# Performance work log

Measured on AMD Instinct MI355X. Metric: run time of the kernel, lower is better.

## Reference

```python
import jax, jax.numpy as jnp
import numpy as np

N = 100000       # nodes
E = 800000       # edges (avg degree 8)
D_IN = 256
D_H = 128
K = 16           # cluster_num
LAMBDA1 = 1.0    # args.alphaH
LAMBDA2 = 0.5    # args.alphaO
GAMMA = 0.1      # args.step_size_gamma


def setup_inputs() -> dict:
    key = jax.random.key(0)
    ks = jax.random.split(key, 8)
    x = jax.random.normal(ks[0], (N, D_IN), jnp.float32)
    edge_index = jax.random.randint(ks[1], (2, E), 0, N, jnp.int32)
    # learned params (glorot-ish small init to keep Gram term numerically tame)
    W1 = jax.random.normal(ks[2], (D_IN, D_H), jnp.float32) * 0.002
    b1 = jnp.zeros((D_H,), jnp.float32)
    W2 = jax.random.normal(ks[3], (D_H, D_H), jnp.float32) * 0.01
    b2 = jnp.zeros((D_H,), jnp.float32)
    Wf = jax.random.normal(ks[4], (D_H, K), jnp.float32) * 0.05
    bf = jnp.zeros((K,), jnp.float32)
    return {"x": x, "edge_index": edge_index, "W1": W1, "b1": b1,
            "W2": W2, "b2": b2, "Wf": Wf, "bf": bf}


def _gcn_norm(edge_index, n):
    # add self loops, symmetric normalization D^-1/2 A D^-1/2 (PyG gcn_norm)
    loops = jnp.arange(n, dtype=edge_index.dtype)
    row = jnp.concatenate([edge_index[0], loops])   # source
    col = jnp.concatenate([edge_index[1], loops])   # target
    w = jnp.ones(row.shape[0], jnp.float32)
    deg = jax.ops.segment_sum(w, col, num_segments=n)
    dinv = jnp.where(deg > 0, jax.lax.rsqrt(jnp.maximum(deg, 1.0)), 0.0)
    return row, col, dinv[row] * w * dinv[col]


def _deprop_layer(x, W, b, row, col, w, n):
    x = x @ W                                               # lin (no bias)
    z = (1.0 - GAMMA * LAMBDA1 + GAMMA * LAMBDA2) * x
    # propagate: gather source features, scale by edge weight, scatter-add to target
    s = GAMMA * LAMBDA1 * jax.ops.segment_sum(w[:, None] * x[row], col, num_segments=n)
    # dense Gram correction: x @ (x^T x), d_h x d_h contraction
    t = GAMMA * LAMBDA2 * (x @ (x.T @ x))
    return jax.nn.relu(z + s - t + b)                       # bias add + ReLU


def reference(x, edge_index, W1, b1, W2, b2, Wf, bf):
    n = x.shape[0]
    row, col, w = _gcn_norm(edge_index, n)  # cached=True -> computed once, reused
    x = _deprop_layer(x, W1, b1, row, col, w, n)
    x = _deprop_layer(x, W2, b2, row, col, w, n)
    logits = x @ Wf + bf                    # fc; dropout is identity in eval mode
    return jax.nn.log_softmax(logits, axis=1)
```

## Files before the change

### kernel.cpp

```cpp
#include <hip/hip_runtime.h>

#define NNODES 100000
#define NEDGES 800000
#define DIN    256
#define DH     128
#define KCLS   16
#define SCAN_NBLK 98
#define GCH 64
#define GRAM_BLK 256

typedef unsigned short u16;
typedef short s16x8 __attribute__((ext_vector_type(8)));
typedef float f32x4 __attribute__((ext_vector_type(4)));

static constexpr float CZ = 0.95f;
static constexpr float CS = 0.10f;
static constexpr float CT = 0.05f;

__device__ __forceinline__ u16 f2b(float f) {
    unsigned u = __builtin_bit_cast(unsigned, f);
    return (u16)((u + 0x7FFFu + ((u >> 16) & 1u)) >> 16);
}
__device__ __forceinline__ float b2f(u16 b) {
    return __builtin_bit_cast(float, ((unsigned)b) << 16);
}
__device__ __forceinline__ s16x8 f2b8(float4 u0, float4 u1) {
    s16x8 v;
    v[0] = (short)f2b(u0.x); v[1] = (short)f2b(u0.y);
    v[2] = (short)f2b(u0.z); v[3] = (short)f2b(u0.w);
    v[4] = (short)f2b(u1.x); v[5] = (short)f2b(u1.y);
    v[6] = (short)f2b(u1.z); v[7] = (short)f2b(u1.w);
    return v;
}


__global__ __launch_bounds__(256) void zero_kernel(int* __restrict__ p) {
    int i = blockIdx.x * 256 + threadIdx.x;
    if (i < NNODES) p[i] = 0;
}

__global__ __launch_bounds__(256) void hist_kernel(const int* __restrict__ col, int* counts) {
    int i = blockIdx.x * 256 + threadIdx.x;
    if (i < NEDGES) atomicAdd(&counts[col[i]], 1);
}

__global__ __launch_bounds__(256) void dinv_kernel(const int* __restrict__ counts, float* dinv) {
    int i = blockIdx.x * 256 + threadIdx.x;
    if (i < NNODES) dinv[i] = rsqrtf((float)(counts[i] + 1));
}

__global__ __launch_bounds__(256) void scan1_kernel(const int* __restrict__ counts,
                                                    int* __restrict__ offsets, int* __restrict__ bsum) {
    __shared__ int ls[256];
    const int b = blockIdx.x, t = threadIdx.x;
    const int base = b * 1024 + t * 4;
    int v0 = (base + 0 < NNODES) ? counts[base + 0] : 0;
    int v1 = (base + 1 < NNODES) ? counts[base + 1] : 0;
    int v2 = (base + 2 < NNODES) ? counts[base + 2] : 0;
    int v3 = (base + 3 < NNODES) ? counts[base + 3] : 0;
    ls[t] = v0 + v1 + v2 + v3;
    __syncthreads();
    for (int off = 1; off < 256; off <<= 1) {
        int v = (t >= off) ? ls[t - off] : 0;
        __syncthreads();
        ls[t] += v;
        __syncthreads();
    }
    int excl = (t == 0) ? 0 : ls[t - 1];
    if (t == 255) bsum[b] = ls[255];
    if (base + 0 < NNODES) offsets[base + 0] = excl;
    if (base + 1 < NNODES) offsets[base + 1] = excl + v0;
    if (base + 2 < NNODES) offsets[base + 2] = excl + v0 + v1;
    if (base + 3 < NNODES) offsets[base + 3] = excl + v0 + v1 + v2;
}

__global__ __launch_bounds__(128) void scan2_kernel(int* bsum) {
    __shared__ int ls[128];
    const int t = threadIdx.x;
    int v = (t < SCAN_NBLK) ? bsum[t] : 0;
    ls[t] = v;
    __syncthreads();
    for (int off = 1; off < 128; off <<= 1) {
        int u = (t >= off) ? ls[t - off] : 0;
        __syncthreads();
        ls[t] += u;
        __syncthreads();
    }
    if (t < SCAN_NBLK) bsum[t] = ls[t] - v;
}

__global__ __launch_bounds__(256) void scan3_kernel(int* __restrict__ offsets, const int* __restrict__ bsum) {
    const int b = blockIdx.x, t = threadIdx.x;
    const int add = bsum[b];
    const int base = b * 1024 + t * 4;
    #pragma unroll
    for (int i = 0; i < 4; ++i)
        if (base + i < NNODES) offsets[base + i] += add;
    if (b == 0 && t == 0) offsets[NNODES] = NEDGES;
}

__global__ __launch_bounds__(256)
void fill_kernel(const int* __restrict__ row, const int* __restrict__ col,
                 const int* __restrict__ offsets, int* __restrict__ cursor,
                 int* __restrict__ eidx) {
    int e = blockIdx.x * 256 + threadIdx.x;
    if (e >= NEDGES) return;
    int c = col[e];
    int p = offsets[c] + atomicAdd(&cursor[c], 1);
    eidx[p] = row[e];
}


template<int KD>
__global__ __launch_bounds__(256)
void tr_w_kernel(const float* __restrict__ W, u16* __restrict__ Wt) {
    int idx = blockIdx.x * 256 + threadIdx.x;
    if (idx < 128 * KD) {
        int c = idx / KD, k = idx % KD;
        Wt[idx] = f2b(W[k * 128 + c]);
    }
}

template<int KD, int EPI, int AF, int WS>
__global__ __launch_bounds__(256, 4)
void mm_bt(const void* __restrict__ Avoid, const u16* __restrict__ Bt,
           u16* __restrict__ Out, const u16* __restrict__ Hb,
           const u16* __restrict__ Sb, const float* __restrict__ bias,
           const float* __restrict__ dinvp, u16* __restrict__ Hs,
           int nrows)
{
    __shared__ __align__(16) u16 as_[2][128 * 40];
    __shared__ __align__(16) u16 bs_[2][128 * 40];
    const int t = threadIdx.x;
    const int w = t >> 6, l = t & 63;
    const int l15 = l & 15, g = l >> 4;
    const int row0 = blockIdx.x * 128;

    const u16*   Ab = (const u16*)Avoid;
    const float* Af = (const float*)Avoid;

    const int sr = t >> 2, so = t & 3;
    int arow[2];
    arow[0] = min(row0 + sr,      nrows - 1);
    arow[1] = min(row0 + 64 + sr, nrows - 1);

    #pragma unroll
    for (int i = 0; i < 2; ++i) {
        s16x8 va;
        if (AF) {
            const float4* p = (const float4*)&Af[(size_t)arow[i] * KD + so * 8];
            va = f2b8(p[0], p[1]);
        } else {
            va = *(const s16x8*)&Ab[(size_t)arow[i] * KD + so * 8];
        }
        s16x8 vb = *(const s16x8*)&Bt[(size_t)(sr + i * 64) * KD + so * 8];
        *(s16x8*)&as_[0][(sr + i * 64) * 40 + so * 8] = va;
        *(s16x8*)&bs_[0][(sr + i * 64) * 40 + so * 8] = vb;
    }
    __syncthreads();

    f32x4 acc[2][8] = {};
    constexpr int NK = KD / 32;

    for (int kc = 0; kc < NK; ++kc) {
        const int buf = kc & 1;
        s16x8 va[2], vb[2];
        const bool pf = (kc + 1 < NK);
        if (pf) {
            const int k0 = (kc + 1) * 32;
            #pragma unroll
            for (int i = 0; i < 2; ++i) {
                if (AF) {
                    const float4* p = (const float4*)&Af[(size_t)arow[i] * KD + k0 + so * 8];
                    va[i] = f2b8(p[0], p[1]);
                } else {
                    va[i] = *(const s16x8*)&Ab[(size_t)arow[i] * KD + k0 + so * 8];
                }
                vb[i] = *(const s16x8*)&Bt[(size_t)(sr + i * 64) * KD + k0 + so * 8];
            }
        }
        s16x8 af0 = *(const s16x8*)&as_[buf][(w * 32 +      l15) * 40 + g * 8];
        s16x8 af1 = *(const s16x8*)&as_[buf][(w * 32 + 16 + l15) * 40 + g * 8];
        #pragma unroll
        for (int n = 0; n < 8; ++n) {
            s16x8 bfr = *(const s16x8*)&bs_[buf][(n * 16 + l15) * 40 + g * 8];
            acc[0][n] = __builtin_amdgcn_mfma_f32_16x16x32_bf16(af0, bfr, acc[0][n], 0, 0, 0);
            acc[1][n] = __builtin_amdgcn_mfma_f32_16x16x32_bf16(af1, bfr, acc[1][n], 0, 0, 0);
        }
        if (pf) {
            #pragma unroll
            for (int i = 0; i < 2; ++i) {
                *(s16x8*)&as_[buf ^ 1][(sr + i * 64) * 40 + so * 8] = va[i];
                *(s16x8*)&bs_[buf ^ 1][(sr + i * 64) * 40 + so * 8] = vb[i];
            }
        }
        __syncthreads();
    }

    float bv[8];
    if (EPI) {
        #pragma unroll
        for (int n = 0; n < 8; ++n) bv[n] = bias[n * 16 + l15];
    }
    #pragma unroll
    for (int m = 0; m < 2; ++m) {
        #pragma unroll
        for (int j = 0; j < 4; ++j) {
            int grow = row0 + w * 32 + m * 16 + g * 4 + j;
            if (grow < nrows) {
                size_t base = (size_t)grow * 128;
                float dv = WS ? dinvp[grow] : 0.f;
                #pragma unroll
                for (int n = 0; n < 8; ++n) {
                    int col = n * 16 + l15;
                    float v = acc[m][n][j];
                    if (EPI) {
                        float h = b2f(Hb[base + col]);
                        float s = b2f(Sb[base + col]);
                        v = fmaxf(CZ * h + CS * s - CT * v + bv[n], 0.f);
                    }
                    Out[base + col] = f2b(v);
                    if (WS) Hs[base + col] = f2b(dv * v);
                }
            }
        }
    }
}

__global__ __launch_bounds__(256)
void gram_gather(const u16* __restrict__ Hb, const u16* __restrict__ Hsb,
                 const float* __restrict__ dinv,
                 const int* __restrict__ offsets, const int* __restrict__ eidx,
                 float* __restrict__ P, u16* __restrict__ Sb, int nrows)
{
    __shared__ __align__(16) u16 ht[128 * GCH];
    const int t = threadIdx.x;

    if (blockIdx.x < GRAM_BLK) {
        const int bid = blockIdx.x;
        const int w = t >> 6, l = t & 63;
        const int l15 = l & 15, g = l >> 4;
        const int nch = (nrows + GCH - 1) / GCH;

        f32x4 acc[2][8] = {};
        const int sr = t >> 2, sq = t & 3;

        for (int ch = bid; ch < nch; ch += GRAM_BLK) {
            {
                int gr = ch * GCH + sr;
                #pragma unroll
                for (int i4 = 0; i4 < 4; ++i4) {
                    int c0 = sq * 32 + i4 * 8;
                    s16x8 v = {};
                    if (gr < nrows) v = *(const s16x8*)&Hb[(size_t)gr * DH + c0];
                    #pragma unroll
                    for (int i = 0; i < 8; ++i) {
                        int c = c0 + i;
                        ht[c * GCH + (sr ^ ((c & 7) << 3))] = (u16)v[i];
                    }
                }
            }
            __syncthreads();
            #pragma unroll
            for (int ks = 0; ks < 2; ++ks) {
                const int kx = (ks * 32 + g * 8) ^ ((l & 7) << 3);
                s16x8 a0 = *(const s16x8*)&ht[(w * 32 +      l15) * GCH + kx];
                s16x8 a1 = *(const s16x8*)&ht[(w * 32 + 16 + l15) * GCH + kx];
                #pragma unroll
                for (int n = 0; n < 8; ++n) {
                    s16x8 bfr = *(const s16x8*)&ht[(n * 16 + l15) * GCH + kx];
                    acc[0][n] = __builtin_amdgcn_mfma_f32_16x16x32_bf16(a0, bfr, acc[0][n], 0, 0, 0);
                    acc[1][n] = __builtin_amdgcn_mfma_f32_16x16x32_bf16(a1, bfr, acc[1][n], 0, 0, 0);
                }
            }
            __syncthreads();
        }

        float* Pb = P + (size_t)bid * (DH * DH);
        #pragma unroll
        for (int m = 0; m < 2; ++m)
            #pragma unroll
            for (int j = 0; j < 4; ++j) {
                int prow = w * 32 + m * 16 + g * 4 + j;
                #pragma unroll
                for (int n = 0; n < 8; ++n)
                    Pb[prow * DH + n * 16 + l15] = acc[m][n][j];
            }
    } else {
        const int grp = t >> 4;
        const int gl  = t & 15;
        const int node = (blockIdx.x - GRAM_BLK) * 16 + grp;
        if (node >= NNODES) return;
        const s16x8* Hs8 = (const s16x8*)Hsb;
        const float d = dinv[node];
        s16x8 hv = Hs8[(size_t)node * 16 + gl];
        float a[8];
        #pragma unroll
        for (int i = 0; i < 8; ++i) a[i] = b2f((u16)hv[i]);
        int p = offsets[node];
        const int e = offsets[node + 1];
        for (; p + 3 < e; p += 4) {
            int r0 = eidx[p], r1 = eidx[p + 1], r2 = eidx[p + 2], r3 = eidx[p + 3];
            s16x8 h0 = Hs8[(size_t)r0 * 16 + gl];
            s16x8 h1 = Hs8[(size_t)r1 * 16 + gl];
            s16x8 h2 = Hs8[(size_t)r2 * 16 + gl];
            s16x8 h3 = Hs8[(size_t)r3 * 16 + gl];
            #pragma unroll
            for (int i = 0; i < 8; ++i) a[i] += b2f((u16)h0[i]);
            #pragma unroll
            for (int i = 0; i < 8; ++i) a[i] += b2f((u16)h1[i]);
            #pragma unroll
            for (int i = 0; i < 8; ++i) a[i] += b2f((u16)h2[i]);
            #pragma unroll
            for (int i = 0; i < 8; ++i) a[i] += b2f((u16)h3[i]);
        }
        for (; p < e; ++p) {
            int r0 = eidx[p];
            s16x8 h0 = Hs8[(size_t)r0 * 16 + gl];
            #pragma unroll
            for (int i = 0; i < 8; ++i) a[i] += b2f((u16)h0[i]);
        }
        s16x8 o;
        #pragma unroll
        for (int i = 0; i < 8; ++i) o[i] = (short)f2b(d * a[i]);
        ((s16x8*)Sb)[(size_t)node * 16 + gl] = o;
    }
}

__global__ __launch_bounds__(256)
void gram_reduce(const float* __restrict__ P, u16* __restrict__ Gb) {
    int idx = blockIdx.x * 256 + threadIdx.x;
    float s = 0.f;
    #pragma unroll 8
    for (int p = 0; p < GRAM_BLK; ++p)
        s += P[(size_t)p * (DH * DH) + idx];
    Gb[idx] = f2b(s);
}

__global__ __launch_bounds__(256)
void fc_mfma(const u16* __restrict__ Xb, const float* __restrict__ Wf,
             const float* __restrict__ bf, float* __restrict__ out, int nrows)
{
    __shared__ __align__(16) u16 wt[KCLS * DH];
    const int t = threadIdx.x;
    const int w = t >> 6, l = t & 63;
    const int l15 = l & 15, g = l >> 4;
    const int row0 = blockIdx.x * 128 + w * 32;

    for (int idx = t; idx < KCLS * DH; idx += 256) {
        int c = idx >> 7, k = idx & 127;
        wt[c * DH + (k ^ ((c & 7) << 3))] = f2b(Wf[k * KCLS + c]);
    }
    __syncthreads();

    int r[2];
    r[0] = min(row0 + l15,      nrows - 1);
    r[1] = min(row0 + 16 + l15, nrows - 1);

    f32x4 acc[2] = {};
    #pragma unroll
    for (int k0 = 0; k0 < DH; k0 += 32) {
        s16x8 a0 = *(const s16x8*)&Xb[(size_t)r[0] * DH + k0 + g * 8];
        s16x8 a1 = *(const s16x8*)&Xb[(size_t)r[1] * DH + k0 + g * 8];
        s16x8 bfr = *(const s16x8*)&wt[l15 * DH + ((k0 + g * 8) ^ ((l & 7) << 3))];
        acc[0] = __builtin_amdgcn_mfma_f32_16x16x32_bf16(a0, bfr, acc[0], 0, 0, 0);
        acc[1] = __builtin_amdgcn_mfma_f32_16x16x32_bf16(a1, bfr, acc[1], 0, 0, 0);
    }

    const float bias = bf[l15];
    #pragma unroll
    for (int m = 0; m < 2; ++m) {
        #pragma unroll
        for (int j = 0; j < 4; ++j) {
            int grow = row0 + m * 16 + g * 4 + j;
            float v = acc[m][j] + bias;
            float mx = v;
            #pragma unroll
            for (int o = 8; o >= 1; o >>= 1)
                mx = fmaxf(mx, __shfl_xor(mx, o));
            float e = expf(v - mx);
            float ssum = e;
            #pragma unroll
            for (int o = 8; o >= 1; o >>= 1)
                ssum += __shfl_xor(ssum, o);
            if (grow < nrows)
                out[(size_t)grow * KCLS + l15] = v - mx - logf(ssum);
        }
    }
}

extern "C" void kernel_launch(void* const* d_in, const int* in_sizes, int n_in,
                              void* d_out, int out_size, void* d_ws, size_t ws_size,
                              hipStream_t stream) {
    const float* x  = (const float*)d_in[0];
    const int*   ei = (const int*)d_in[1];
    const float* W1 = (const float*)d_in[2];
    const float* b1 = (const float*)d_in[3];
    const float* W2 = (const float*)d_in[4];
    const float* b2 = (const float*)d_in[5];
    const float* Wf = (const float*)d_in[6];
    const float* bf = (const float*)d_in[7];
    float* out = (float*)d_out;

    const int* row = ei;
    const int* col = ei + NEDGES;

    float* dinv    = (float*)d_ws;
    float* P       = dinv + 102400;
    int*   counts  = (int*)(P + (size_t)GRAM_BLK * DH * DH);
    int*   offsets = counts + 102400;
    int*   bsum    = offsets + 102656;
    int*   eidx    = bsum + 128;
    u16*   B0b     = (u16*)(eidx + NEDGES);
    u16*   B1b     = B0b + (size_t)NNODES * DH;
    u16*   Sb      = B1b + (size_t)NNODES * DH;
    u16*   Hsb     = Sb + (size_t)NNODES * DH;
    u16*   W1t     = Hsb + (size_t)NNODES * DH;
    u16*   W2t     = W1t + 128 * DIN;
    u16*   Gb      = W2t + 128 * DH;

    dim3 b256(256);
    const int gN  = (NNODES + 255) / 256;
    const int gE  = (NEDGES + 255) / 256;
    const int gMM = (NNODES + 127) / 128;
    const int gGG = GRAM_BLK + (NNODES + 15) / 16;

    zero_kernel<<<gN, b256, 0, stream>>>(counts);
    hist_kernel<<<gE, b256, 0, stream>>>(col, counts);
    dinv_kernel<<<gN, b256, 0, stream>>>(counts, dinv);
    scan1_kernel<<<SCAN_NBLK, b256, 0, stream>>>(counts, offsets, bsum);
    scan2_kernel<<<1, 128, 0, stream>>>(bsum);
    scan3_kernel<<<SCAN_NBLK, b256, 0, stream>>>(offsets, bsum);
    zero_kernel<<<gN, b256, 0, stream>>>(counts);
    fill_kernel<<<gE, b256, 0, stream>>>(row, col, offsets, counts, eidx);
    tr_w_kernel<DIN><<<(128 * DIN + 255) / 256, b256, 0, stream>>>(W1, W1t);
    tr_w_kernel<DH><<<(128 * DH + 255) / 256, b256, 0, stream>>>(W2, W2t);

    mm_bt<DIN, 0, 1, 1><<<gMM, b256, 0, stream>>>(x, W1t, B0b, nullptr, nullptr, nullptr, dinv, Hsb, NNODES);
    gram_gather<<<gGG, b256, 0, stream>>>(B0b, Hsb, dinv, offsets, eidx, P, Sb, NNODES);
    gram_reduce<<<64, b256, 0, stream>>>(P, Gb);
    mm_bt<DH, 1, 0, 0><<<gMM, b256, 0, stream>>>(B0b, Gb, B1b, B0b, Sb, b1, nullptr, nullptr, NNODES);

    mm_bt<DH, 0, 0, 1><<<gMM, b256, 0, stream>>>(B1b, W2t, B0b, nullptr, nullptr, nullptr, dinv, Hsb, NNODES);
    gram_gather<<<gGG, b256, 0, stream>>>(B0b, Hsb, dinv, offsets, eidx, P, Sb, NNODES);
    gram_reduce<<<64, b256, 0, stream>>>(P, Gb);
    mm_bt<DH, 1, 0, 0><<<gMM, b256, 0, stream>>>(B0b, Gb, B1b, B0b, Sb, b2, nullptr, nullptr, NNODES);

    fc_mfma<<<gMM, b256, 0, stream>>>(B1b, Wf, bf, out, NNODES);
}
```

Baseline: 319.4 us.

## Deepen GEMM prefetch to two register stages ahead of LDS compute

Restructures the tiled MFMA GEMM main loop so global loads run two K-chunks ahead, alternating between two register staging sets and two LDS buffers. The fp32-to-bf16 conversion moves from load time to LDS-write time, so raw float4 loads can stay in flight longer. The aim is to hide global memory latency behind more MFMA work, at the cost of extra registers that may lower occupancy. The loop assumes NK is even.

```diff
diff --git a/kernel.cpp b/kernel.cpp
--- a/kernel.cpp
+++ b/kernel.cpp
@@ -144,56 +144,59 @@
     arow[0] = min(row0 + sr,      nrows - 1);
     arow[1] = min(row0 + 64 + sr, nrows - 1);
 
-    #pragma unroll
-    for (int i = 0; i < 2; ++i) {
-        s16x8 va;
-        if (AF) {
-            const float4* p = (const float4*)&Af[(size_t)arow[i] * KD + so * 8];
-            va = f2b8(p[0], p[1]);
-        } else {
-            va = *(const s16x8*)&Ab[(size_t)arow[i] * KD + so * 8];
-        }
-        s16x8 vb = *(const s16x8*)&Bt[(size_t)(sr + i * 64) * KD + so * 8];
-        *(s16x8*)&as_[0][(sr + i * 64) * 40 + so * 8] = va;
-        *(s16x8*)&bs_[0][(sr + i * 64) * 40 + so * 8] = vb;
-    }
-    __syncthreads();
-
     f32x4 acc[2][8] = {};
     constexpr int NK = KD / 32;
 
-    for (int kc = 0; kc < NK; ++kc) {
-        const int buf = kc & 1;
-        s16x8 va[2], vb[2];
-        const bool pf = (kc + 1 < NK);
-        if (pf) {
-            const int k0 = (kc + 1) * 32;
-            #pragma unroll
-            for (int i = 0; i < 2; ++i) {
-                if (AF) {
-                    const float4* p = (const float4*)&Af[(size_t)arow[i] * KD + k0 + so * 8];
-                    va[i] = f2b8(p[0], p[1]);
-                } else {
-                    va[i] = *(const s16x8*)&Ab[(size_t)arow[i] * KD + k0 + so * 8];
-                }
-                vb[i] = *(const s16x8*)&Bt[(size_t)(sr + i * 64) * KD + k0 + so * 8];
+    float4 paf0[2][2], paf1[2][2];
+    s16x8  pa0[2],     pa1[2];
+    s16x8  pb0[2],     pb1[2];
+
+    auto load_chunk = [&](int kc_, float4 (&pafS)[2][2], s16x8 (&paS)[2], s16x8 (&pbS)[2]) {
+        const int k0 = kc_ * 32;
+        #pragma unroll
+        for (int i = 0; i < 2; ++i) {
+            if (AF) {
+                const float4* p = (const float4*)&Af[(size_t)arow[i] * KD + k0 + so * 8];
+                pafS[i][0] = p[0];
+                pafS[i][1] = p[1];
+            } else {
+                paS[i] = *(const s16x8*)&Ab[(size_t)arow[i] * KD + k0 + so * 8];
             }
-        }
-        s16x8 af0 = *(const s16x8*)&as_[buf][(w * 32 +      l15) * 40 + g * 8];
-        s16x8 af1 = *(const s16x8*)&as_[buf][(w * 32 + 16 + l15) * 40 + g * 8];
+            pbS[i] = *(const s16x8*)&Bt[(size_t)(sr + i * 64) * KD + k0 + so * 8];
+        }
+    };
+    auto write_chunk = [&](int buf_, float4 (&pafS)[2][2], s16x8 (&paS)[2], s16x8 (&pbS)[2]) {
+        #pragma unroll
+        for (int i = 0; i < 2; ++i) {
+            s16x8 va = AF ? f2b8(pafS[i][0], pafS[i][1]) : paS[i];
+            *(s16x8*)&as_[buf_][(sr + i * 64) * 40 + so * 8] = va;
+            *(s16x8*)&bs_[buf_][(sr + i * 64) * 40 + so * 8] = pbS[i];
+        }
+    };
+    auto compute = [&](int buf_) {
+        s16x8 af0 = *(const s16x8*)&as_[buf_][(w * 32 +      l15) * 40 + g * 8];
+        s16x8 af1 = *(const s16x8*)&as_[buf_][(w * 32 + 16 + l15) * 40 + g * 8];
         #pragma unroll
         for (int n = 0; n < 8; ++n) {
-            s16x8 bfr = *(const s16x8*)&bs_[buf][(n * 16 + l15) * 40 + g * 8];
+            s16x8 bfr = *(const s16x8*)&bs_[buf_][(n * 16 + l15) * 40 + g * 8];
             acc[0][n] = __builtin_amdgcn_mfma_f32_16x16x32_bf16(af0, bfr, acc[0][n], 0, 0, 0);
             acc[1][n] = __builtin_amdgcn_mfma_f32_16x16x32_bf16(af1, bfr, acc[1][n], 0, 0, 0);
         }
-        if (pf) {
-            #pragma unroll
-            for (int i = 0; i < 2; ++i) {
-                *(s16x8*)&as_[buf ^ 1][(sr + i * 64) * 40 + so * 8] = va[i];
-                *(s16x8*)&bs_[buf ^ 1][(sr + i * 64) * 40 + so * 8] = vb[i];
-            }
-        }
+    };
+
+    load_chunk(0, paf0, pa0, pb0);
+    write_chunk(0, paf0, pa0, pb0);
+    load_chunk(1, paf1, pa1, pb1);
+    __syncthreads();
+
+    for (int kc = 0; kc < NK; kc += 2) {
+        if (kc + 2 < NK) load_chunk(kc + 2, paf0, pa0, pb0);
+        compute(0);
+        write_chunk(1, paf1, pa1, pb1);
+        __syncthreads();
+        if (kc + 3 < NK) load_chunk(kc + 3, paf1, pa1, pb1);
+        compute(1);
+        if (kc + 2 < NK) write_chunk(0, paf0, pa0, pb0);
         __syncthreads();
     }
 
```

After: 321.8 us. No clear change (+0.7%).
